# Performance work log

Hardware: AMD Instinct MI355X
Metric: run time of the kernel (lower is better)

The kernel has to match this reference:

```python
import jax, jax.numpy as jnp
import numpy as np

B, M, N, D = 2, 2048, 2048, 2048
N_H, D_H, D_R = 16, 128, 64
THETA = 1000000.0
SCALE = 1.0 / np.sqrt(D_H + D_R)


def build_rope_cache(seq_len, dim, theta):
    freqs = 1.0 / theta ** (jnp.arange(0, dim, 2, dtype=jnp.float32) / dim)
    t = jnp.arange(seq_len, dtype=jnp.float32)
    freqs = jnp.outer(t, freqs)  # (S, dim//2)
    cos = jnp.repeat(jnp.cos(freqs), 2, axis=-1)  # (S, dim)
    sin = jnp.repeat(jnp.sin(freqs), 2, axis=-1)
    return cos, sin


def apply_rope(x, cos, sin):
    # x: (..., S, dim); cos/sin broadcastable (S, dim)
    x_rot = jnp.stack([-x[..., 1::2], x[..., ::2]], axis=-1).reshape(x.shape)
    return x * cos + x_rot * sin


def setup_inputs() -> dict:
    key = jax.random.key(0)
    ks = jax.random.split(key, 8)
    std = 0.02
    return {
        "query": jax.random.normal(ks[0], (B, M, D), jnp.float32),
        "key_value": jax.random.normal(ks[1], (B, N, D), jnp.float32),
        "W_QC": jax.random.normal(ks[2], (N_H * D_H, D), jnp.float32) * std,
        "W_KC": jax.random.normal(ks[3], (N_H * D_H, D), jnp.float32) * std,
        "W_QR": jax.random.normal(ks[4], (N_H * D_R, D), jnp.float32) * std,
        "W_KR": jax.random.normal(ks[5], (N_H * D_R, D), jnp.float32) * std,
        "W_V": jax.random.normal(ks[6], (N_H * D_H, D), jnp.float32) * std,
        "W_O": jax.random.normal(ks[7], (D, N_H * D_H), jnp.float32) * std,
    }


def reference(query, key_value, W_QC, W_KC, W_QR, W_KR, W_V, W_O):
    # projections: torch Linear is x @ W.T
    Q_C = (query @ W_QC.T).reshape(B, M, N_H, D_H).transpose(0, 2, 1, 3)  # (B,H,M,dh)
    K_C = (key_value @ W_KC.T).reshape(B, N, N_H, D_H).transpose(0, 2, 1, 3)
    Q_R = (query @ W_QR.T).reshape(B, M, N_H, D_R).transpose(0, 2, 1, 3)  # (B,H,M,dR)
    K_R = (key_value @ W_KR.T).reshape(B, N, N_H, D_R).transpose(0, 2, 1, 3)
    cos, sin = build_rope_cache(max(M, N), D_R, THETA)
    Q_R = apply_rope(Q_R, cos[:M], sin[:M])
    K_R = apply_rope(K_R, cos[:N], sin[:N])
    scores = (jnp.einsum('bhmd,bhnd->bhmn', Q_C, K_C)
              + jnp.einsum('bhmr,bhnr->bhmn', Q_R, K_R)) * SCALE
    attn = jax.nn.softmax(scores, axis=-1)
    V = (key_value @ W_V.T).reshape(B, N, N_H, D_H).transpose(0, 2, 1, 3)
    out = jnp.einsum('bhmn,bhnd->bhmd', attn, V)  # (B,H,M,dh)
    out = out.transpose(0, 2, 1, 3).reshape(B, M, N_H * D_H)
    return out @ W_O.T
```

## Files before the change

### kernel.cpp

```cpp
#include <hip/hip_runtime.h>
#include <hip/hip_bf16.h>

typedef unsigned short u16;
typedef unsigned int u32;
typedef unsigned long long u64;
typedef __attribute__((ext_vector_type(8))) short short8;
typedef __attribute__((ext_vector_type(4))) float floatx4;

#if __has_builtin(__builtin_amdgcn_exp2f)
#define EXP2F(x) __builtin_amdgcn_exp2f(x)
#else
#define EXP2F(x) exp2f(x)
#endif

#define QSCALE (0.07216878364870323f * 1.4426950408889634f)
#define ROPE_C 0.62286151779f

__device__ __forceinline__ u16 f2b(float f) {
    unsigned int x = __builtin_bit_cast(unsigned int, f);
    unsigned int r = (x + 0x7fffu + ((x >> 16) & 1u)) >> 16;
    return (u16)r;
}
__device__ __forceinline__ u32 pk2(float a, float b) {
    return (u32)f2b(a) | ((u32)f2b(b) << 16);
}
__device__ __forceinline__ void async16(const void* g, void* l) {
    __builtin_amdgcn_global_load_lds(
        (const __attribute__((address_space(1))) void*)g,
        (__attribute__((address_space(3))) void*)l, 16, 0, 0);
}

struct CastArgs {
    const float* src[8];
    u16* dst[8];
    float scale[8];
    int startblk[8];
};

__global__ void cast_all_k(CastArgs a)
{
    const int bid = blockIdx.x;
    int s = 0;
#pragma unroll
    for (int i = 1; i < 8; ++i) s += (bid >= a.startblk[i]);
    const long idx = ((long)(bid - a.startblk[s]) * 256 + threadIdx.x) * 4;
    const float4 v = *(const float4*)(a.src[s] + idx);
    const float sc = a.scale[s];
    const u64 pk = (u64)pk2(v.x * sc, v.y * sc)
                 | ((u64)pk2(v.z * sc, v.w * sc) << 32);
    *(u64*)(a.dst[s] + idx) = pk;
}

template<int EPI>
__global__ void __launch_bounds__(256, 3)
gemm_bt(const u16* __restrict__ A, const u16* __restrict__ Bw,
        void* __restrict__ out0, u16* __restrict__ out1, u16* __restrict__ out2,
        int K)
{
    __shared__ u16 As[128 * 64];
    __shared__ u16 Bs[128 * 64];
    const int t = threadIdx.x;
    const int w = t >> 6;
    const int lane = t & 63;
    const int lq = lane >> 4, lr = lane & 15;

    const int nwg = gridDim.x;
    const int id = blockIdx.x;
    const int wid = (id & 7) * (nwg >> 3) + (id >> 3);
    const long tileM = (long)(wid & 31) << 7;
    const long tileN = (long)(wid >> 5) << 7;

    const int wm = (w >> 1) * 64, wn = (w & 1) * 64;

    const floatx4 fzero = {0.f, 0.f, 0.f, 0.f};
    floatx4 acc[4][4];
#pragma unroll
    for (int i = 0; i < 4; ++i)
#pragma unroll
        for (int j = 0; j < 4; ++j) acc[i][j] = fzero;

    for (int k0 = 0; k0 < K; k0 += 64) {
#pragma unroll
        for (int r = 0; r < 4; ++r) {
            const int c = r * 256 + t;
            const int row = c >> 3, cc = c & 7;
            const int gcol = ((cc ^ (row & 7)) << 3);
            async16(A + (tileM + row) * (long)K + k0 + gcol, (char*)As + c * 16);
        }
#pragma unroll
        for (int r = 0; r < 4; ++r) {
            const int c = r * 256 + t;
            const int row = c >> 3, cc = c & 7;
            const int gcol = ((cc ^ (row & 7)) << 3);
            async16(Bw + (tileN + row) * (long)K + k0 + gcol, (char*)Bs + c * 16);
        }
        __builtin_amdgcn_s_waitcnt(0);
        __syncthreads();
#pragma unroll
        for (int kk = 0; kk < 2; ++kk) {
            short8 af[4], bfr[4];
#pragma unroll
            for (int i = 0; i < 4; ++i) {
                const int row = wm + 16 * i + lr;
                const int cc = (kk * 4 + lq) ^ (row & 7);
                af[i] = *(const short8*)(As + row * 64 + cc * 8);
            }
#pragma unroll
            for (int j = 0; j < 4; ++j) {
                const int row = wn + 16 * j + lr;
                const int cc = (kk * 4 + lq) ^ (row & 7);
                bfr[j] = *(const short8*)(Bs + row * 64 + cc * 8);
            }
            __builtin_amdgcn_s_setprio(1);
#pragma unroll
            for (int i = 0; i < 4; ++i)
#pragma unroll
                for (int j = 0; j < 4; ++j)
                    acc[i][j] = __builtin_amdgcn_mfma_f32_16x16x32_bf16(
                        af[i], bfr[j], acc[i][j], 0, 0, 0);
            __builtin_amdgcn_s_setprio(0);
        }
        __syncthreads();
    }

    const bool isV    = (EPI == 1) && (tileN >= 3072);
    const bool isRope = (EPI != 2) && !isV && (tileN >= 2048);

#pragma unroll
    for (int i = 0; i < 4; ++i) {
#pragma unroll
        for (int j = 0; j < 4; ++j) {
            const long row0 = tileM + wm + 16 * i + 4 * lq;
            const long col  = tileN + wn + 16 * j + lr;
            if (EPI == 2) {
#pragma unroll
                for (int r = 0; r < 4; ++r)
                    ((float*)out0)[(row0 + r) * 2048 + col] = acc[i][j][r];
            } else if (isV) {
                const u32 lo = pk2(acc[i][j][0], acc[i][j][1]);
                const u32 hi = pk2(acc[i][j][2], acc[i][j][3]);
                const long bb = row0 >> 11;
                u16* dst = out2 + ((bb * 2048 + (col - 3072)) << 11) + (row0 & 2047);
                *(uint2*)dst = make_uint2(lo, hi);
            } else if (isRope) {
                const int jj = ((int)col & 63) >> 1;
                const float freq = EXP2F(-ROPE_C * (float)jj);
#pragma unroll
                for (int r = 0; r < 4; ++r) {
                    const float v = acc[i][j][r];
                    const float vp = __shfl_xor(v, 1, 64);
                    const long row = row0 + r;
                    float sn, cs;
                    __sincosf((float)(row & 2047) * freq, &sn, &cs);
                    const float o = (col & 1) ? (v * cs + vp * sn) : (v * cs - vp * sn);
                    out1[row * 1024 + (col - 2048)] = f2b(o);
                }
            } else {
#pragma unroll
                for (int r = 0; r < 4; ++r)
                    ((u16*)out0)[(row0 + r) * 2048 + col] = f2b(acc[i][j][r]);
            }
        }
    }
}

__global__ void __launch_bounds__(256, 2)
flash_attn(const u16* __restrict__ QC, const u16* __restrict__ QR,
           const u16* __restrict__ KC, const u16* __restrict__ KR,
           const u16* __restrict__ VT, u16* __restrict__ Obuf)
{
    __shared__ u16 KV_s[64 * 128 + 64 * 64];
    __shared__ u16 VT_s[128 * 64];

    const int t = threadIdx.x;
    const int w = t >> 6;
    const int lane = t & 63;
    const int lq = lane >> 4, lr = lane & 15;
    const int bx = blockIdx.x, by = blockIdx.y;
    const int h  = ((bx & 7) << 1) | (by & 1);
    const int qx = ((bx >> 3) << 3) | (by >> 1);
    const int mbase = qx * 128 + w * 32;
    const int b = blockIdx.z;

    short8 aq[2][6];
#pragma unroll
    for (int i = 0; i < 2; ++i) {
        const long m = mbase + 16 * i + lr;
        const u16* qc = QC + ((long)b * 2048 + m) * 2048 + h * 128;
        const u16* qr = QR + ((long)b * 2048 + m) * 1024 + h * 64;
#pragma unroll
        for (int kc = 0; kc < 4; ++kc) aq[i][kc]     = *(const short8*)(qc + kc * 32 + lq * 8);
#pragma unroll
        for (int kc = 0; kc < 2; ++kc) aq[i][4 + kc] = *(const short8*)(qr + kc * 32 + lq * 8);
    }

    const floatx4 fzero = {0.f, 0.f, 0.f, 0.f};
    float mst[2], lst[2];
    floatx4 oacc[2][8];
#pragma unroll
    for (int i = 0; i < 2; ++i) {
        mst[i] = -1e30f; lst[i] = 0.f;
#pragma unroll
        for (int jn = 0; jn < 8; ++jn) oacc[i][jn] = fzero;
    }

    const u16* kc_g = KC + ((long)b * 2048) * 2048 + h * 128;
    const u16* kr_g = KR + ((long)b * 2048) * 1024 + h * 64;
    const u16* vt_g = VT + ((long)(b * 16 + h) * 128) * 2048;

    for (int kt = 0; kt < 32; ++kt) {
#pragma unroll
        for (int r = 0; r < 4; ++r) {
            const int c = r * 256 + t;
            const int krow = c >> 4, cc = c & 15;
            const int gc = cc ^ (krow & 7);
            async16(kc_g + (long)(kt * 64 + krow) * 2048 + gc * 8, (char*)KV_s + c * 16);
        }
#pragma unroll
        for (int r = 0; r < 2; ++r) {
            const int c = r * 256 + t;
            const int krow = c >> 3, cc = c & 7;
            const int gc = cc ^ (krow & 7);
            async16(kr_g + (long)(kt * 64 + krow) * 1024 + gc * 8, (char*)KV_s + 16384 + c * 16);
        }
#pragma unroll
        for (int r = 0; r < 4; ++r) {
            const int c = r * 256 + t;
            const int drow = c >> 3, cc = c & 7;
            const int gc = cc ^ (drow & 7);
            async16(vt_g + (long)drow * 2048 + kt * 64 + gc * 8, (char*)VT_s + c * 16);
        }
        __builtin_amdgcn_s_waitcnt(0);
        __syncthreads();

        floatx4 sT[4][2];
#pragma unroll
        for (int j = 0; j < 4; ++j)
#pragma unroll
            for (int i = 0; i < 2; ++i) sT[j][i] = fzero;
#pragma unroll
        for (int kc = 0; kc < 6; ++kc) {
            short8 kf[4];
#pragma unroll
            for (int j = 0; j < 4; ++j) {
                const int krow = 16 * j + lr;
                if (kc < 4) {
                    const int cc = (4 * kc + lq) ^ (krow & 7);
                    kf[j] = *(const short8*)(KV_s + krow * 128 + cc * 8);
                } else {
                    const int cc = (4 * (kc - 4) + lq) ^ (krow & 7);
                    kf[j] = *(const short8*)(KV_s + 8192 + krow * 64 + cc * 8);
                }
            }
            __builtin_amdgcn_s_setprio(1);
#pragma unroll
            for (int j = 0; j < 4; ++j)
#pragma unroll
                for (int i = 0; i < 2; ++i)
                    sT[j][i] = __builtin_amdgcn_mfma_f32_16x16x32_bf16(
                        kf[j], aq[i][kc], sT[j][i], 0, 0, 0);
            __builtin_amdgcn_s_setprio(0);
        }

        float rmax[2];
#pragma unroll
        for (int i = 0; i < 2; ++i) {
            float a0 = fmaxf(fmaxf(sT[0][i][0], sT[0][i][1]), fmaxf(sT[0][i][2], sT[0][i][3]));
            float a1 = fmaxf(fmaxf(sT[1][i][0], sT[1][i][1]), fmaxf(sT[1][i][2], sT[1][i][3]));
            float a2 = fmaxf(fmaxf(sT[2][i][0], sT[2][i][1]), fmaxf(sT[2][i][2], sT[2][i][3]));
            float a3 = fmaxf(fmaxf(sT[3][i][0], sT[3][i][1]), fmaxf(sT[3][i][2], sT[3][i][3]));
            rmax[i] = fmaxf(fmaxf(a0, a1), fmaxf(a2, a3));
        }
#pragma unroll
        for (int i = 0; i < 2; ++i) {
            rmax[i] = fmaxf(rmax[i], __shfl_xor(rmax[i], 16, 64));
            rmax[i] = fmaxf(rmax[i], __shfl_xor(rmax[i], 32, 64));
        }

        const int upd = (rmax[0] > mst[0] + 8.f) | (rmax[1] > mst[1] + 8.f);
        if (__any(upd)) {
#pragma unroll
            for (int i = 0; i < 2; ++i) {
                const float mnew = fmaxf(mst[i], rmax[i]);
                const float alpha = EXP2F(mst[i] - mnew);
                mst[i] = mnew;
                lst[i] *= alpha;
#pragma unroll
                for (int jn = 0; jn < 8; ++jn)
#pragma unroll
                    for (int r = 0; r < 4; ++r) oacc[i][jn][r] *= alpha;
            }
        }

        float rsum[2] = {0.f, 0.f};
#pragma unroll
        for (int j = 0; j < 4; ++j)
#pragma unroll
            for (int i = 0; i < 2; ++i)
#pragma unroll
                for (int r = 0; r < 4; ++r) {
                    const float p = EXP2F(sT[j][i][r] - mst[i]);
                    sT[j][i][r] = p;
                    rsum[i] += p;
                }
#pragma unroll
        for (int i = 0; i < 2; ++i) {
            rsum[i] += __shfl_xor(rsum[i], 16, 64);
            rsum[i] += __shfl_xor(rsum[i], 32, 64);
            lst[i] += rsum[i];
        }

        __syncthreads();

        u16* pw = KV_s + w * 2048;
#pragma unroll
        for (int i = 0; i < 2; ++i)
#pragma unroll
            for (int j = 0; j < 4; ++j) {
                const int row = 16 * i + lr;
                const int c8 = (2 * j + (lq >> 1)) ^ (row & 7);
                const u32 d0 = pk2(sT[j][i][0], sT[j][i][1]);
                const u32 d1 = pk2(sT[j][i][2], sT[j][i][3]);
                *(uint2*)(pw + row * 64 + c8 * 8 + 4 * (lq & 1)) = make_uint2(d0, d1);
            }

#pragma unroll
        for (int kc = 0; kc < 2; ++kc) {
            short8 ap[2];
#pragma unroll
            for (int i = 0; i < 2; ++i) {
                const int row = 16 * i + lr;
                ap[i] = *(const short8*)(pw + row * 64 + (((4 * kc + lq) ^ (row & 7)) << 3));
            }
            __builtin_amdgcn_s_setprio(1);
#pragma unroll
            for (int jn = 0; jn < 8; ++jn) {
                const int drow = 16 * jn + lr;
                const int cc = (4 * kc + lq) ^ (drow & 7);
                const short8 bv = *(const short8*)(VT_s + drow * 64 + cc * 8);
#pragma unroll
                for (int i = 0; i < 2; ++i)
                    oacc[i][jn] = __builtin_amdgcn_mfma_f32_16x16x32_bf16(
                        bv, ap[i], oacc[i][jn], 0, 0, 0);
            }
            __builtin_amdgcn_s_setprio(0);
        }
        __syncthreads();
    }

#pragma unroll
    for (int i = 0; i < 2; ++i) {
        const float rl = 1.0f / lst[i];
        const long row = (long)b * 2048 + mbase + 16 * i + lr;
#pragma unroll
        for (int jn = 0; jn < 8; ++jn) {
            const u32 lo = pk2(oacc[i][jn][0] * rl, oacc[i][jn][1] * rl);
            const u32 hi = pk2(oacc[i][jn][2] * rl, oacc[i][jn][3] * rl);
            u16* dst = Obuf + row * 2048 + h * 128 + 16 * jn + 4 * lq;
            *(uint2*)dst = make_uint2(lo, hi);
        }
    }
}

extern "C" void kernel_launch(void* const* d_in, const int* in_sizes, int n_in,
                              void* d_out, int out_size, void* d_ws, size_t ws_size,
                              hipStream_t stream)
{
    (void)in_sizes; (void)n_in; (void)out_size; (void)ws_size;

    u16* p = (u16*)d_ws;
    u16* qbf   = p; p += 8388608;
    u16* kvbf  = p; p += 8388608;
    u16* wqall = p; p += 6291456;
    u16* wkvall= p; p += 10485760;
    u16* wob   = p; p += 4194304;
    u16* QCb   = p; p += 8388608;
    u16* QRb   = p; p += 4194304;
    u16* KCb   = p; p += 8388608;
    u16* KRb   = p; p += 4194304;
    u16* VTb   = p; p += 8388608;
    u16* Ob    = p; p += 8388608;

    CastArgs a;
    a.src[0] = (const float*)d_in[0]; a.dst[0] = qbf;               a.scale[0] = QSCALE;
    a.src[1] = (const float*)d_in[1]; a.dst[1] = kvbf;              a.scale[1] = 1.f;
    a.src[2] = (const float*)d_in[2]; a.dst[2] = wqall;             a.scale[2] = 1.f;
    a.src[3] = (const float*)d_in[3]; a.dst[3] = wkvall;            a.scale[3] = 1.f;
    a.src[4] = (const float*)d_in[4]; a.dst[4] = wqall + 4194304;   a.scale[4] = 1.f;
    a.src[5] = (const float*)d_in[5]; a.dst[5] = wkvall + 4194304;  a.scale[5] = 1.f;
    a.src[6] = (const float*)d_in[6]; a.dst[6] = wkvall + 6291456;  a.scale[6] = 1.f;
    a.src[7] = (const float*)d_in[7]; a.dst[7] = wob;               a.scale[7] = 1.f;
    const int blks[8] = {8192, 8192, 4096, 4096, 2048, 2048, 4096, 4096};
    int acc = 0;
    for (int i = 0; i < 8; ++i) { a.startblk[i] = acc; acc += blks[i]; }

    cast_all_k<<<acc, 256, 0, stream>>>(a);

    gemm_bt<0><<<32 * 24, 256, 0, stream>>>(qbf,  wqall,  QCb, QRb, nullptr, 2048);
    gemm_bt<1><<<32 * 40, 256, 0, stream>>>(kvbf, wkvall, KCb, KRb, VTb,     2048);

    flash_attn<<<dim3(16, 16, 2), 256, 0, stream>>>(QCb, QRb, KCb, KRb, VTb, Ob);

    gemm_bt<2><<<32 * 16, 256, 0, stream>>>(Ob, wob, d_out, nullptr, nullptr, 2048);
}
```

Baseline: 485.1 us.

## Double-buffer K/V tiles in flash attention to overlap loads with compute

Merges the K, K-rope and V^T shared-memory tiles into one buffer and keeps two copies of it. The global-to-LDS async loads for tile kt+1 are issued before tile kt is computed. A partial vmcnt wait (waiting only for the previous stage's loads) replaces the full waitcnt(0) plus __syncthreads, with sched_barrier fences around raw s_barrier calls. This aims to hide global memory latency behind the MFMA and softmax work. The cost is doubling LDS per block to 80KB, which must still fit two blocks per CU, and the correctness depends on the hard-coded count of ten loads per stage.

```diff
diff --git a/kernel.cpp b/kernel.cpp
--- a/kernel.cpp
+++ b/kernel.cpp
@@ -169,8 +169,7 @@
            const u16* __restrict__ KC, const u16* __restrict__ KR,
            const u16* __restrict__ VT, u16* __restrict__ Obuf)
 {
-    __shared__ u16 KV_s[64 * 128 + 64 * 64];
-    __shared__ u16 VT_s[128 * 64];
+    __shared__ u16 BUF[2][20480];
 
     const int t = threadIdx.x;
     const int w = t >> 6;
@@ -208,30 +207,44 @@
     const u16* kr_g = KR + ((long)b * 2048) * 1024 + h * 64;
     const u16* vt_g = VT + ((long)(b * 16 + h) * 128) * 2048;
 
-    for (int kt = 0; kt < 32; ++kt) {
+    auto stage = [&](int bf, int kt) {
+        char* base = (char*)&BUF[bf][0];
 #pragma unroll
         for (int r = 0; r < 4; ++r) {
             const int c = r * 256 + t;
             const int krow = c >> 4, cc = c & 15;
             const int gc = cc ^ (krow & 7);
-            async16(kc_g + (long)(kt * 64 + krow) * 2048 + gc * 8, (char*)KV_s + c * 16);
+            async16(kc_g + (long)(kt * 64 + krow) * 2048 + gc * 8, base + c * 16);
         }
 #pragma unroll
         for (int r = 0; r < 2; ++r) {
             const int c = r * 256 + t;
             const int krow = c >> 3, cc = c & 7;
             const int gc = cc ^ (krow & 7);
-            async16(kr_g + (long)(kt * 64 + krow) * 1024 + gc * 8, (char*)KV_s + 16384 + c * 16);
+            async16(kr_g + (long)(kt * 64 + krow) * 1024 + gc * 8, base + 16384 + c * 16);
         }
 #pragma unroll
         for (int r = 0; r < 4; ++r) {
             const int c = r * 256 + t;
             const int drow = c >> 3, cc = c & 7;
             const int gc = cc ^ (drow & 7);
-            async16(vt_g + (long)drow * 2048 + kt * 64 + gc * 8, (char*)VT_s + c * 16);
-        }
-        __builtin_amdgcn_s_waitcnt(0);
-        __syncthreads();
+            async16(vt_g + (long)drow * 2048 + kt * 64 + gc * 8, base + 24576 + c * 16);
+        }
+    };
+
+    stage(0, 0);
+
+    for (int kt = 0; kt < 32; ++kt) {
+        const int cur = kt & 1;
+        if (kt + 1 < 32) stage(cur ^ 1, kt + 1);
+        __builtin_amdgcn_sched_barrier(0);
+        if (kt + 1 < 32) { asm volatile("s_waitcnt vmcnt(10)" ::: "memory"); }
+        else             { asm volatile("s_waitcnt vmcnt(0)"  ::: "memory"); }
+        __builtin_amdgcn_sched_barrier(0);
+        __builtin_amdgcn_s_barrier();
+        __builtin_amdgcn_sched_barrier(0);
+
+        u16* kv = &BUF[cur][0];
 
         floatx4 sT[4][2];
 #pragma unroll
@@ -246,10 +259,10 @@
                 const int krow = 16 * j + lr;
                 if (kc < 4) {
                     const int cc = (4 * kc + lq) ^ (krow & 7);
-                    kf[j] = *(const short8*)(KV_s + krow * 128 + cc * 8);
+                    kf[j] = *(const short8*)(kv + krow * 128 + cc * 8);
                 } else {
                     const int cc = (4 * (kc - 4) + lq) ^ (krow & 7);
-                    kf[j] = *(const short8*)(KV_s + 8192 + krow * 64 + cc * 8);
+                    kf[j] = *(const short8*)(kv + 8192 + krow * 64 + cc * 8);
                 }
             }
             __builtin_amdgcn_s_setprio(1);
@@ -310,9 +323,11 @@
             lst[i] += rsum[i];
         }
 
-        __syncthreads();
-
-        u16* pw = KV_s + w * 2048;
+        __builtin_amdgcn_sched_barrier(0);
+        __builtin_amdgcn_s_barrier();
+        __builtin_amdgcn_sched_barrier(0);
+
+        u16* pw = kv + w * 2048;
 #pragma unroll
         for (int i = 0; i < 2; ++i)
 #pragma unroll
@@ -337,7 +352,7 @@
             for (int jn = 0; jn < 8; ++jn) {
                 const int drow = 16 * jn + lr;
                 const int cc = (4 * kc + lq) ^ (drow & 7);
-                const short8 bv = *(const short8*)(VT_s + drow * 64 + cc * 8);
+                const short8 bv = *(const short8*)(kv + 12288 + drow * 64 + cc * 8);
 #pragma unroll
                 for (int i = 0; i < 2; ++i)
                     oacc[i][jn] = __builtin_amdgcn_mfma_f32_16x16x32_bf16(
@@ -345,7 +360,10 @@
             }
             __builtin_amdgcn_s_setprio(0);
         }
-        __syncthreads();
+
+        __builtin_amdgcn_sched_barrier(0);
+        __builtin_amdgcn_s_barrier();
+        __builtin_amdgcn_sched_barrier(0);
     }
 
 #pragma unroll
```

New measurement: 481.2 us. Within noise of the previous version (-0.8%).
